# Performance work log

Hardware: AMD Instinct MI355X
Metric: run time of the kernel (lower is better)

The kernel has to match this reference:

```python
import jax, jax.numpy as jnp
import numpy as np

N, E = 50000, 800000
F_IN, E_DIM, D, H = 128, 64, 64, 4  # per-head channels D, heads H; concat=False -> out dim D
GROUPS = 16
EPS = 1e-5


def _p(key, shape, scale):
    return (jax.random.normal(key, shape, dtype=jnp.float32) * scale)


def setup_inputs() -> dict:
    key = jax.random.key(0)
    ks = jax.random.split(key, 40)
    inp = {
        "x": jax.random.normal(ks[0], (N, F_IN), dtype=jnp.float32),
        "edge_index": jax.random.randint(ks[1], (2, E), 0, N, dtype=jnp.int64),
        "edge_attr": jax.random.normal(ks[2], (E, E_DIM), dtype=jnp.float32),
    }
    # TransformerConv params, layer i: Wq/Wk/Wv [in, H*D] (+bias), We [E_DIM, H*D] (no bias),
    # Wskip [in, D] (+bias).  Layer 1 in=F_IN, layers 2/3 in=D.
    idx = 3
    for i, fin in zip((1, 2, 3), (F_IN, D, D)):
        s = 1.0 / np.sqrt(fin)
        se = 1.0 / np.sqrt(E_DIM)
        inp[f"Wq{i}"] = _p(ks[idx + 0], (fin, H * D), s)
        inp[f"bq{i}"] = jnp.zeros((H * D,), jnp.float32)
        inp[f"Wk{i}"] = _p(ks[idx + 1], (fin, H * D), s)
        inp[f"bk{i}"] = jnp.zeros((H * D,), jnp.float32)
        inp[f"Wv{i}"] = _p(ks[idx + 2], (fin, H * D), s)
        inp[f"bv{i}"] = jnp.zeros((H * D,), jnp.float32)
        inp[f"We{i}"] = _p(ks[idx + 3], (E_DIM, H * D), se)
        inp[f"Wskip{i}"] = _p(ks[idx + 4], (fin, D), s)
        inp[f"bskip{i}"] = jnp.zeros((D,), jnp.float32)
        idx += 5
    inp["gn_w"] = jnp.ones((D,), jnp.float32)
    inp["gn_b"] = jnp.zeros((D,), jnp.float32)
    return inp


def transformer_conv(x, src, dst, edge_attr, Wq, bq, Wk, bk, Wv, bv, We, Wskip, bskip):
    n = x.shape[0]
    q = (x @ Wq + bq).reshape(n, H, D)
    k = (x @ Wk + bk).reshape(n, H, D)
    v = (x @ Wv + bv).reshape(n, H, D)
    e = (edge_attr @ We).reshape(-1, H, D)  # [E,H,D]
    k_e = k[src] + e                          # edge-level key
    v_e = v[src] + e                          # edge-level value
    alpha = jnp.einsum('ehd,ehd->eh', q[dst], k_e) / np.sqrt(D)  # [E,H]
    # segment softmax over incoming edges of each dst node
    amax = jax.ops.segment_max(alpha, dst, num_segments=n)
    amax = jnp.where(jnp.isfinite(amax), amax, 0.0)
    ex = jnp.exp(alpha - amax[dst])
    denom = jax.ops.segment_sum(ex, dst, num_segments=n)
    attn = ex / (denom[dst] + 1e-16)
    out = jax.ops.segment_sum(attn[:, :, None] * v_e, dst, num_segments=n)  # [N,H,D]
    out = out.mean(axis=1)                     # concat=False -> mean over heads
    return out + (x @ Wskip + bskip)           # root_weight skip


def group_norm(x, w, b):
    n, c = x.shape
    xg = x.reshape(n, GROUPS, c // GROUPS)
    mu = xg.mean(axis=2, keepdims=True)
    var = xg.var(axis=2, keepdims=True)
    xn = ((xg - mu) * jax.lax.rsqrt(var + EPS)).reshape(n, c)
    return xn * w + b


def reference(x, edge_index, edge_attr,
              Wq1, bq1, Wk1, bk1, Wv1, bv1, We1, Wskip1, bskip1,
              Wq2, bq2, Wk2, bk2, Wv2, bv2, We2, Wskip2, bskip2,
              Wq3, bq3, Wk3, bk3, Wv3, bv3, We3, Wskip3, bskip3,
              gn_w, gn_b):
    src, dst = edge_index[0], edge_index[1]
    layers = [
        (Wq1, bq1, Wk1, bk1, Wv1, bv1, We1, Wskip1, bskip1),
        (Wq2, bq2, Wk2, bk2, Wv2, bv2, We2, Wskip2, bskip2),
        (Wq3, bq3, Wk3, bk3, Wv3, bv3, We3, Wskip3, bskip3),
    ]
    h = x
    for prm in layers:
        h = transformer_conv(h, src, dst, edge_attr, *prm)
        h = group_norm(h, gn_w, gn_b)
        h = jax.nn.gelu(h, approximate=False)
    return h
```

## Files before the change

kernel.cpp:

```cpp
#include <hip/hip_runtime.h>
#include <math.h>

#define NN 50000
#define NE 800000
#define NCOLS 1088

typedef long long i64;

__global__ void detect_i64(const int* __restrict__ ei32, int* __restrict__ flag) {
  int i = blockIdx.x * blockDim.x + threadIdx.x;
  if (i < 2048) {
    if (ei32[2 * i + 1] != 0) atomicOr(flag, 1);
  }
}

__global__ void extract_edges(const void* __restrict__ ei, const int* __restrict__ flag,
                              int* __restrict__ src32, int* __restrict__ dst32, int ne) {
  int is32 = *flag;
  int i = blockIdx.x * blockDim.x + threadIdx.x;
  int st = gridDim.x * blockDim.x;
  if (is32) {
    const int* p = (const int*)ei;
    for (; i < ne; i += st) { src32[i] = p[i]; dst32[i] = p[ne + i]; }
  } else {
    const i64* p = (const i64*)ei;
    for (; i < ne; i += st) { src32[i] = (int)p[i]; dst32[i] = (int)p[ne + i]; }
  }
}

__global__ void hist_kernel(const int* __restrict__ dst, int* __restrict__ deg, int ne) {
  int i = blockIdx.x * blockDim.x + threadIdx.x;
  int st = gridDim.x * blockDim.x;
  for (; i < ne; i += st) atomicAdd(&deg[dst[i]], 1);
}

__global__ void scan_kernel(const int* __restrict__ deg, int* __restrict__ row_ptr, int n) {
  __shared__ int buf[1024];
  int t = threadIdx.x;
  int carry = 0;
  if (t == 0) row_ptr[0] = 0;
  for (int base = 0; base < n; base += 1024) {
    int v = (base + t < n) ? deg[base + t] : 0;
    buf[t] = v;
    __syncthreads();
    for (int off = 1; off < 1024; off <<= 1) {
      int x = (t >= off) ? buf[t - off] : 0;
      __syncthreads();
      buf[t] += x;
      __syncthreads();
    }
    if (base + t < n) row_ptr[base + t + 1] = carry + buf[t];
    carry += buf[1023];
    __syncthreads();
  }
}

__global__ void scatter_kernel(const int* __restrict__ src, const int* __restrict__ dst,
                               const int* __restrict__ row_ptr, int* __restrict__ cursor,
                               int* __restrict__ src_sorted, int* __restrict__ eid_sorted, int ne) {
  int i = blockIdx.x * blockDim.x + threadIdx.x;
  int st = gridDim.x * blockDim.x;
  for (; i < ne; i += st) {
    int d = dst[i];
    int pos = row_ptr[d] + atomicAdd(&cursor[d], 1);
    src_sorted[pos] = src[i];
    eid_sorted[pos] = i;
  }
}

__global__ void sort_lists(const int* __restrict__ row_ptr, int* __restrict__ src_sorted,
                           int* __restrict__ eid_sorted, int n) {
  int node = blockIdx.x * blockDim.x + threadIdx.x;
  if (node >= n) return;
  int beg = row_ptr[node], end = row_ptr[node + 1];
  for (int a = beg + 1; a < end; ++a) {
    int e = eid_sorted[a], s = src_sorted[a];
    int b = a - 1;
    while (b >= beg && eid_sorted[b] > e) {
      eid_sorted[b + 1] = eid_sorted[b];
      src_sorted[b + 1] = src_sorted[b];
      --b;
    }
    eid_sorted[b + 1] = e; src_sorted[b + 1] = s;
  }
}

__global__ void prep_wt(const float* __restrict__ Wq, const float* __restrict__ Wk,
                        const float* __restrict__ Wv, const float* __restrict__ We,
                        const float* __restrict__ Wsk, float* __restrict__ Wt, int fin) {
  int i = blockIdx.x * blockDim.x + threadIdx.x;
  if (i >= NCOLS * fin) return;
  int col = i / fin, k = i % fin;
  float val;
  if (col < 768) {
    const float* W = (col < 256) ? Wq : (col < 512) ? Wk : Wv;
    val = W[k * 256 + (col & 255)];
  } else if (col < 1024) {
    int idx = col - 768; int h = idx >> 6, ce = idx & 63;
    float a = 0.f;
    for (int d = 0; d < 64; ++d) a += Wq[k * 256 + h * 64 + d] * We[ce * 256 + h * 64 + d];
    val = a;
  } else {
    val = Wsk[k * 64 + (col - 1024)];
  }
  Wt[(size_t)col * fin + k] = val;
}

__global__ void prep_bias(const float* __restrict__ bq, const float* __restrict__ bk,
                          const float* __restrict__ bv, const float* __restrict__ We,
                          const float* __restrict__ bsk, float* __restrict__ bb) {
  int col = blockIdx.x * blockDim.x + threadIdx.x;
  if (col >= NCOLS) return;
  float val;
  if (col < 768) {
    const float* b = (col < 256) ? bq : (col < 512) ? bk : bv;
    val = b[col & 255];
  } else if (col < 1024) {
    int idx = col - 768; int h = idx >> 6, ce = idx & 63;
    float a = 0.f;
    for (int d = 0; d < 64; ++d) a += bq[h * 64 + d] * We[ce * 256 + h * 64 + d];
    val = a;
  } else {
    val = bsk[col - 1024];
  }
  bb[col] = val;
}

__global__ __launch_bounds__(256) void node_gemm_f32(
    const float* __restrict__ X, const float* __restrict__ Wt, const float* __restrict__ bb,
    float* __restrict__ q_tab, float* __restrict__ k_tab, float* __restrict__ v_tab,
    float* __restrict__ qt_tab, float* __restrict__ skip_tab, int n, int fin) {
  __shared__ __align__(16) float Xs[128][68];
  __shared__ __align__(16) float Ws[64][68];
  int tid = threadIdx.x;
  int tx = tid & 15, ty = tid >> 4;
  int m0 = blockIdx.x * 128, c0 = blockIdx.y * 64;
  float acc[8][4];
  #pragma unroll
  for (int i = 0; i < 8; ++i)
    #pragma unroll
    for (int j = 0; j < 4; ++j) acc[i][j] = 0.f;

  for (int k0 = 0; k0 < fin; k0 += 64) {
    #pragma unroll
    for (int p = 0; p < 8; ++p) {
      int r = ty + 16 * p;
      float4 xv = make_float4(0.f, 0.f, 0.f, 0.f);
      if (m0 + r < n) xv = *(const float4*)&X[(size_t)(m0 + r) * fin + k0 + tx * 4];
      *(float4*)&Xs[r][tx * 4] = xv;
    }
    #pragma unroll
    for (int p = 0; p < 4; ++p) {
      int r = ty + 16 * p;
      float4 wv = *(const float4*)&Wt[(size_t)(c0 + r) * fin + k0 + tx * 4];
      *(float4*)&Ws[r][tx * 4] = wv;
    }
    __syncthreads();
    #pragma unroll 4
    for (int kk = 0; kk < 64; kk += 4) {
      float4 a[8], b[4];
      #pragma unroll
      for (int i = 0; i < 8; ++i) a[i] = *(const float4*)&Xs[ty + 16 * i][kk];
      #pragma unroll
      for (int j = 0; j < 4; ++j) b[j] = *(const float4*)&Ws[tx + 16 * j][kk];
      #pragma unroll
      for (int i = 0; i < 8; ++i)
        #pragma unroll
        for (int j = 0; j < 4; ++j) {
          acc[i][j] = fmaf(a[i].x, b[j].x, acc[i][j]);
          acc[i][j] = fmaf(a[i].y, b[j].y, acc[i][j]);
          acc[i][j] = fmaf(a[i].z, b[j].z, acc[i][j]);
          acc[i][j] = fmaf(a[i].w, b[j].w, acc[i][j]);
        }
    }
    __syncthreads();
  }
  #pragma unroll
  for (int j = 0; j < 4; ++j) {
    int col = c0 + tx + 16 * j;
    float bias = bb[col];
    #pragma unroll
    for (int i = 0; i < 8; ++i) {
      int row = m0 + ty + 16 * i;
      if (row >= n) continue;
      float val = acc[i][j] + bias;
      if (col < 256)       q_tab[(size_t)row * 256 + col] = val;
      else if (col < 512)  k_tab[(size_t)row * 256 + col - 256] = val;
      else if (col < 768)  v_tab[(size_t)row * 256 + col - 512] = val;
      else if (col < 1024) qt_tab[(size_t)row * 256 + col - 768] = val;
      else                 skip_tab[(size_t)row * 64 + col - 1024] = val;
    }
  }
}

__global__ __launch_bounds__(256, 6) void attn_kernel_f32(
    const int* __restrict__ row_ptr, const int* __restrict__ src_sorted,
    const int* __restrict__ eid_sorted, const float* __restrict__ ea,
    const float* __restrict__ q_tab, const float* __restrict__ k_tab,
    const float* __restrict__ v_tab, const float* __restrict__ qt_tab,
    const float* __restrict__ skip_tab, const float* __restrict__ west,
    const float* __restrict__ gnw, const float* __restrict__ gnb,
    float* __restrict__ out, int n) {
  int tid = threadIdx.x;
  int wave = tid >> 6, lane = tid & 63;
  int node = blockIdx.x * 4 + wave;
  if (node >= n) return;
  int h = lane >> 4;
  int foff = h * 16 + (lane & 15);
  const float4* q4p = (const float4*)q_tab;
  const float4* t4p = (const float4*)qt_tab;
  const float4* k4p = (const float4*)k_tab;
  const float4* v4p = (const float4*)v_tab;
  const float4* e4p = (const float4*)ea;
  const float4* w4p = (const float4*)west;

  float4 q4 = q4p[(size_t)node * 64 + foff];
  float4 t4 = t4p[(size_t)node * 64 + foff];

  float m = -INFINITY, s = 0.f;
  float4 av = make_float4(0.f, 0.f, 0.f, 0.f);
  float4 aw = make_float4(0.f, 0.f, 0.f, 0.f);

  int beg = row_ptr[node], end = row_ptr[node + 1];
  float4 kp, vp, ep;
  if (beg < end) {
    int sidx = src_sorted[beg], eid = eid_sorted[beg];
    kp = k4p[(size_t)sidx * 64 + foff];
    vp = v4p[(size_t)sidx * 64 + foff];
    ep = e4p[(size_t)eid * 16 + (lane & 15)];
  }
  for (int j = beg; j < end; ++j) {
    float4 kc = kp, vc = vp, ec = ep;
    if (j + 1 < end) {
      int sidx = src_sorted[j + 1], eid = eid_sorted[j + 1];
      kp = k4p[(size_t)sidx * 64 + foff];
      vp = v4p[(size_t)sidx * 64 + foff];
      ep = e4p[(size_t)eid * 16 + (lane & 15)];
    }
    float p = q4.x * kc.x + q4.y * kc.y + q4.z * kc.z + q4.w * kc.w
            + t4.x * ec.x + t4.y * ec.y + t4.z * ec.z + t4.w * ec.w;
    p += __shfl_xor(p, 1);
    p += __shfl_xor(p, 2);
    p += __shfl_xor(p, 4);
    p += __shfl_xor(p, 8);
    p *= 0.125f;
    float d_ = p - m;
    float e_ = __expf(-fabsf(d_));
    float sc = d_ > 0.f ? e_ : 1.f;
    float pp = d_ > 0.f ? 1.f : e_;
    m = fmaxf(m, p);
    s = s * sc + pp;
    av.x = av.x * sc + pp * vc.x; av.y = av.y * sc + pp * vc.y;
    av.z = av.z * sc + pp * vc.z; av.w = av.w * sc + pp * vc.w;
    aw.x = aw.x * sc + pp * ec.x; aw.y = aw.y * sc + pp * ec.y;
    aw.z = aw.z * sc + pp * ec.z; aw.w = aw.w * sc + pp * ec.w;
  }
  float inv = s > 0.f ? 1.f / s : 0.f;
  float4 avn = make_float4(av.x * inv, av.y * inv, av.z * inv, av.w * inv);
  float4 awn = make_float4(aw.x * inv, aw.y * inv, aw.z * inv, aw.w * inv);

  float4 post = make_float4(0.f, 0.f, 0.f, 0.f);
  int gbase = h << 4;
  #pragma unroll 4
  for (int ce4 = 0; ce4 < 16; ++ce4) {
    int srcl = gbase | ce4;
    float wa = __shfl(awn.x, srcl);
    float wb = __shfl(awn.y, srcl);
    float wc = __shfl(awn.z, srcl);
    float wd = __shfl(awn.w, srcl);
    float4 w0 = w4p[(size_t)(ce4 * 4 + 0) * 64 + foff];
    float4 w1 = w4p[(size_t)(ce4 * 4 + 1) * 64 + foff];
    float4 w2 = w4p[(size_t)(ce4 * 4 + 2) * 64 + foff];
    float4 w3 = w4p[(size_t)(ce4 * 4 + 3) * 64 + foff];
    post.x = fmaf(wa, w0.x, post.x); post.y = fmaf(wa, w0.y, post.y);
    post.z = fmaf(wa, w0.z, post.z); post.w = fmaf(wa, w0.w, post.w);
    post.x = fmaf(wb, w1.x, post.x); post.y = fmaf(wb, w1.y, post.y);
    post.z = fmaf(wb, w1.z, post.z); post.w = fmaf(wb, w1.w, post.w);
    post.x = fmaf(wc, w2.x, post.x); post.y = fmaf(wc, w2.y, post.y);
    post.z = fmaf(wc, w2.z, post.z); post.w = fmaf(wc, w2.w, post.w);
    post.x = fmaf(wd, w3.x, post.x); post.y = fmaf(wd, w3.y, post.y);
    post.z = fmaf(wd, w3.z, post.z); post.w = fmaf(wd, w3.w, post.w);
  }

  float4 tot = make_float4(avn.x + post.x, avn.y + post.y, avn.z + post.z, avn.w + post.w);
  tot.x += __shfl_xor(tot.x, 16); tot.y += __shfl_xor(tot.y, 16);
  tot.z += __shfl_xor(tot.z, 16); tot.w += __shfl_xor(tot.w, 16);
  tot.x += __shfl_xor(tot.x, 32); tot.y += __shfl_xor(tot.y, 32);
  tot.z += __shfl_xor(tot.z, 32); tot.w += __shfl_xor(tot.w, 32);

  int srcl = lane >> 2;
  float va = __shfl(tot.x, srcl);
  float vb = __shfl(tot.y, srcl);
  float vc2 = __shfl(tot.z, srcl);
  float vd = __shfl(tot.w, srcl);
  float v01 = (lane & 1) ? vb : va;
  float v23 = (lane & 1) ? vd : vc2;
  float hsum = (lane & 2) ? v23 : v01;

  float val = 0.25f * hsum + skip_tab[(size_t)node * 64 + lane];
  float sm = val + __shfl_xor(val, 1);
  sm += __shfl_xor(sm, 2);
  float mu = sm * 0.25f;
  float dv = val - mu;
  float vq = dv * dv;
  float v2 = vq + __shfl_xor(vq, 1);
  v2 += __shfl_xor(v2, 2);
  float xn = dv * rsqrtf(v2 * 0.25f + 1e-5f);
  float y = xn * gnw[lane] + gnb[lane];
  float g = 0.5f * y * (1.0f + erff(y * 0.70710678118654752f));
  out[(size_t)node * 64 + lane] = g;
}

extern "C" void kernel_launch(void* const* d_in, const int* in_sizes, int n_in,
                              void* d_out, int out_size, void* d_ws, size_t ws_size,
                              hipStream_t stream) {
  (void)in_sizes; (void)n_in;
  const float* x = (const float*)d_in[0];
  const void* ei = d_in[1];
  const float* ea = (const float*)d_in[2];
  const float *Wq[3], *bq[3], *Wk[3], *bk[3], *Wv[3], *bv[3], *We[3], *Wsk[3], *bsk[3];
  for (int L = 0; L < 3; ++L) {
    int b = 3 + 9 * L;
    Wq[L] = (const float*)d_in[b + 0]; bq[L] = (const float*)d_in[b + 1];
    Wk[L] = (const float*)d_in[b + 2]; bk[L] = (const float*)d_in[b + 3];
    Wv[L] = (const float*)d_in[b + 4]; bv[L] = (const float*)d_in[b + 5];
    We[L] = (const float*)d_in[b + 6]; Wsk[L] = (const float*)d_in[b + 7];
    bsk[L] = (const float*)d_in[b + 8];
  }
  const float* gnw = (const float*)d_in[30];
  const float* gnb = (const float*)d_in[31];

  char* p = (char*)d_ws;
  auto alloc = [&](size_t bytes) -> void* {
    void* r = (void*)p;
    p += (bytes + 255) & ~(size_t)255;
    return r;
  };
  float* q_tab = (float*)alloc((size_t)NN * 256 * 4);
  float* k_tab = (float*)alloc((size_t)NN * 256 * 4);
  float* v_tab = (float*)alloc((size_t)NN * 256 * 4);
  float* qt_tab = (float*)alloc((size_t)NN * 256 * 4);
  float* skip_tab = (float*)alloc((size_t)NN * 64 * 4);
  float* h_buf = (float*)alloc((size_t)NN * 64 * 4);
  int* row_ptr = (int*)alloc((size_t)(NN + 1) * 4);
  int* deg = (int*)alloc((size_t)NN * 4);
  int* cursor = (int*)alloc((size_t)NN * 4);
  int* src_sorted = (int*)alloc((size_t)NE * 4);
  int* eid_sorted = (int*)alloc((size_t)NE * 4);
  int* src32 = (int*)alloc((size_t)NE * 4);
  int* dst32 = (int*)alloc((size_t)NE * 4);
  int* flag = (int*)alloc(256);
  float* Wt[3]; float* bb[3];
  Wt[0] = (float*)alloc((size_t)NCOLS * 128 * 4);
  Wt[1] = (float*)alloc((size_t)NCOLS * 64 * 4);
  Wt[2] = (float*)alloc((size_t)NCOLS * 64 * 4);
  for (int L = 0; L < 3; ++L) bb[L] = (float*)alloc((size_t)NCOLS * 4);

  if ((size_t)(p - (char*)d_ws) > ws_size) {
    hipMemsetAsync(d_out, 0, (size_t)out_size * 4, stream);
    return;
  }

  hipMemsetAsync(deg, 0, (size_t)NN * 4, stream);
  hipMemsetAsync(cursor, 0, (size_t)NN * 4, stream);
  hipMemsetAsync(flag, 0, 4, stream);

  detect_i64<<<8, 256, 0, stream>>>((const int*)ei, flag);
  extract_edges<<<2048, 256, 0, stream>>>(ei, flag, src32, dst32, NE);

  hist_kernel<<<2048, 256, 0, stream>>>(dst32, deg, NE);
  scan_kernel<<<1, 1024, 0, stream>>>(deg, row_ptr, NN);
  scatter_kernel<<<2048, 256, 0, stream>>>(src32, dst32, row_ptr, cursor, src_sorted, eid_sorted, NE);
  sort_lists<<<(NN + 255) / 256, 256, 0, stream>>>(row_ptr, src_sorted, eid_sorted, NN);

  for (int L = 0; L < 3; ++L) {
    int fin = (L == 0) ? 128 : 64;
    prep_wt<<<(NCOLS * fin + 255) / 256, 256, 0, stream>>>(Wq[L], Wk[L], Wv[L], We[L], Wsk[L], Wt[L], fin);
    prep_bias<<<(NCOLS + 255) / 256, 256, 0, stream>>>(bq[L], bk[L], bv[L], We[L], bsk[L], bb[L]);
  }

  const float* hin = x;
  int ngroups = (NN + 3) / 4;
  for (int L = 0; L < 3; ++L) {
    int fin = (L == 0) ? 128 : 64;
    dim3 g((NN + 127) / 128, 17);
    node_gemm_f32<<<g, 256, 0, stream>>>(hin, Wt[L], bb[L], q_tab, k_tab, v_tab, qt_tab, skip_tab, NN, fin);
    attn_kernel_f32<<<ngroups, 256, 0, stream>>>(
        row_ptr, src_sorted, eid_sorted, ea, q_tab, k_tab, v_tab, qt_tab,
        skip_tab, We[L], gnw, gnb,
        (L == 2) ? (float*)d_out : h_buf, NN);
    hin = h_buf;
  }
}
```

Before: 1.778 ms.

## Interleave K/V and Q/QT tables and deepen edge gather prefetch to four

Node projections are now stored interleaved per row: K and V share one 2KB row, and Q and the transformed query share another. The aim is that each gathered source node's K and V fall in adjacent memory, which should improve locality for the random gathers. The attention loop now processes two edges per iteration with four edges of loads in flight, exposing more memory-level parallelism. The cost is higher register pressure under the 6-waves launch bound, which could cause spills or lower occupancy.

```diff
diff --git a/kernel.cpp b/kernel.cpp
--- a/kernel.cpp
+++ b/kernel.cpp
@@ -128,8 +128,8 @@
 
 __global__ __launch_bounds__(256) void node_gemm_f32(
     const float* __restrict__ X, const float* __restrict__ Wt, const float* __restrict__ bb,
-    float* __restrict__ q_tab, float* __restrict__ k_tab, float* __restrict__ v_tab,
-    float* __restrict__ qt_tab, float* __restrict__ skip_tab, int n, int fin) {
+    float* __restrict__ qq_tab, float* __restrict__ kv_tab,
+    float* __restrict__ skip_tab, int n, int fin) {
   __shared__ __align__(16) float Xs[128][68];
   __shared__ __align__(16) float Ws[64][68];
   int tid = threadIdx.x;
@@ -184,11 +184,10 @@
       int row = m0 + ty + 16 * i;
       if (row >= n) continue;
       float val = acc[i][j] + bias;
-      if (col < 256)       q_tab[(size_t)row * 256 + col] = val;
-      else if (col < 512)  k_tab[(size_t)row * 256 + col - 256] = val;
-      else if (col < 768)  v_tab[(size_t)row * 256 + col - 512] = val;
-      else if (col < 1024) qt_tab[(size_t)row * 256 + col - 768] = val;
-      else                 skip_tab[(size_t)row * 64 + col - 1024] = val;
+      if (col < 256)        qq_tab[(size_t)row * 512 + col] = val;
+      else if (col < 768)   kv_tab[(size_t)row * 512 + col - 256] = val;
+      else if (col < 1024)  qq_tab[(size_t)row * 512 + col - 512] = val;
+      else                  skip_tab[(size_t)row * 64 + col - 1024] = val;
     }
   }
 }
@@ -196,8 +195,7 @@
 __global__ __launch_bounds__(256, 6) void attn_kernel_f32(
     const int* __restrict__ row_ptr, const int* __restrict__ src_sorted,
     const int* __restrict__ eid_sorted, const float* __restrict__ ea,
-    const float* __restrict__ q_tab, const float* __restrict__ k_tab,
-    const float* __restrict__ v_tab, const float* __restrict__ qt_tab,
+    const float* __restrict__ qq_tab, const float* __restrict__ kv_tab,
     const float* __restrict__ skip_tab, const float* __restrict__ west,
     const float* __restrict__ gnw, const float* __restrict__ gnb,
     float* __restrict__ out, int n) {
@@ -207,54 +205,79 @@
   if (node >= n) return;
   int h = lane >> 4;
   int foff = h * 16 + (lane & 15);
-  const float4* q4p = (const float4*)q_tab;
-  const float4* t4p = (const float4*)qt_tab;
-  const float4* k4p = (const float4*)k_tab;
-  const float4* v4p = (const float4*)v_tab;
+  int eoff = lane & 15;
+  const float4* qq4 = (const float4*)qq_tab;
+  const float4* kv4 = (const float4*)kv_tab;
   const float4* e4p = (const float4*)ea;
   const float4* w4p = (const float4*)west;
 
-  float4 q4 = q4p[(size_t)node * 64 + foff];
-  float4 t4 = t4p[(size_t)node * 64 + foff];
+  float4 q4 = qq4[(size_t)node * 128 + foff];
+  float4 t4 = qq4[(size_t)node * 128 + 64 + foff];
 
   float m = -INFINITY, s = 0.f;
   float4 av = make_float4(0.f, 0.f, 0.f, 0.f);
   float4 aw = make_float4(0.f, 0.f, 0.f, 0.f);
 
   int beg = row_ptr[node], end = row_ptr[node + 1];
-  float4 kp, vp, ep;
-  if (beg < end) {
-    int sidx = src_sorted[beg], eid = eid_sorted[beg];
-    kp = k4p[(size_t)sidx * 64 + foff];
-    vp = v4p[(size_t)sidx * 64 + foff];
-    ep = e4p[(size_t)eid * 16 + (lane & 15)];
-  }
-  for (int j = beg; j < end; ++j) {
-    float4 kc = kp, vc = vp, ec = ep;
-    if (j + 1 < end) {
-      int sidx = src_sorted[j + 1], eid = eid_sorted[j + 1];
-      kp = k4p[(size_t)sidx * 64 + foff];
-      vp = v4p[(size_t)sidx * 64 + foff];
-      ep = e4p[(size_t)eid * 16 + (lane & 15)];
-    }
-    float p = q4.x * kc.x + q4.y * kc.y + q4.z * kc.z + q4.w * kc.w
-            + t4.x * ec.x + t4.y * ec.y + t4.z * ec.z + t4.w * ec.w;
-    p += __shfl_xor(p, 1);
-    p += __shfl_xor(p, 2);
-    p += __shfl_xor(p, 4);
-    p += __shfl_xor(p, 8);
-    p *= 0.125f;
-    float d_ = p - m;
-    float e_ = __expf(-fabsf(d_));
-    float sc = d_ > 0.f ? e_ : 1.f;
-    float pp = d_ > 0.f ? 1.f : e_;
-    m = fmaxf(m, p);
-    s = s * sc + pp;
-    av.x = av.x * sc + pp * vc.x; av.y = av.y * sc + pp * vc.y;
-    av.z = av.z * sc + pp * vc.z; av.w = av.w * sc + pp * vc.w;
-    aw.x = aw.x * sc + pp * ec.x; aw.y = aw.y * sc + pp * ec.y;
-    aw.z = aw.z * sc + pp * ec.z; aw.w = aw.w * sc + pp * ec.w;
-  }
+
+#define LOADE(idx, K, V, E)                                   \
+  {                                                           \
+    int s_ = src_sorted[idx];                                 \
+    int e_ = eid_sorted[idx];                                 \
+    K = kv4[(size_t)s_ * 128 + foff];                         \
+    V = kv4[(size_t)s_ * 128 + 64 + foff];                    \
+    E = e4p[(size_t)e_ * 16 + eoff];                          \
+  }
+
+#define ONLINE1(p, V, E)                                      \
+  {                                                           \
+    float d_ = (p) - m;                                       \
+    float e_ = __expf(-fabsf(d_));                            \
+    float sc = d_ > 0.f ? e_ : 1.f;                           \
+    float pp = d_ > 0.f ? 1.f : e_;                           \
+    m = fmaxf(m, (p));                                        \
+    s = s * sc + pp;                                          \
+    av.x = av.x * sc + pp * V.x; av.y = av.y * sc + pp * V.y; \
+    av.z = av.z * sc + pp * V.z; av.w = av.w * sc + pp * V.w; \
+    aw.x = aw.x * sc + pp * E.x; aw.y = aw.y * sc + pp * E.y; \
+    aw.z = aw.z * sc + pp * E.z; aw.w = aw.w * sc + pp * E.w; \
+  }
+
+  float4 Ka, Va, Ea, Kb, Vb, Eb, Kc, Vc, Ec, Kd, Vd, Ed;
+  int j = beg;
+  if (j     < end) LOADE(j,     Ka, Va, Ea);
+  if (j + 1 < end) LOADE(j + 1, Kb, Vb, Eb);
+  if (j + 2 < end) LOADE(j + 2, Kc, Vc, Ec);
+  if (j + 3 < end) LOADE(j + 3, Kd, Vd, Ed);
+
+  for (; j + 1 < end; j += 2) {
+    float4 K0 = Ka, V0 = Va, E0 = Ea, K1 = Kb, V1 = Vb, E1 = Eb;
+    Ka = Kc; Va = Vc; Ea = Ec; Kb = Kd; Vb = Vd; Eb = Ed;
+    if (j + 4 < end) LOADE(j + 4, Kc, Vc, Ec);
+    if (j + 5 < end) LOADE(j + 5, Kd, Vd, Ed);
+    float p0 = q4.x * K0.x + q4.y * K0.y + q4.z * K0.z + q4.w * K0.w
+             + t4.x * E0.x + t4.y * E0.y + t4.z * E0.z + t4.w * E0.w;
+    float p1 = q4.x * K1.x + q4.y * K1.y + q4.z * K1.z + q4.w * K1.w
+             + t4.x * E1.x + t4.y * E1.y + t4.z * E1.z + t4.w * E1.w;
+    p0 += __shfl_xor(p0, 1);  p1 += __shfl_xor(p1, 1);
+    p0 += __shfl_xor(p0, 2);  p1 += __shfl_xor(p1, 2);
+    p0 += __shfl_xor(p0, 4);  p1 += __shfl_xor(p1, 4);
+    p0 += __shfl_xor(p0, 8);  p1 += __shfl_xor(p1, 8);
+    p0 *= 0.125f; p1 *= 0.125f;
+    ONLINE1(p0, V0, E0);
+    ONLINE1(p1, V1, E1);
+  }
+  if (j < end) {
+    float p0 = q4.x * Ka.x + q4.y * Ka.y + q4.z * Ka.z + q4.w * Ka.w
+             + t4.x * Ea.x + t4.y * Ea.y + t4.z * Ea.z + t4.w * Ea.w;
+    p0 += __shfl_xor(p0, 1);
+    p0 += __shfl_xor(p0, 2);
+    p0 += __shfl_xor(p0, 4);
+    p0 += __shfl_xor(p0, 8);
+    p0 *= 0.125f;
+    ONLINE1(p0, Va, Ea);
+  }
+
   float inv = s > 0.f ? 1.f / s : 0.f;
   float4 avn = make_float4(av.x * inv, av.y * inv, av.z * inv, av.w * inv);
   float4 awn = make_float4(aw.x * inv, aw.y * inv, aw.z * inv, aw.w * inv);
@@ -336,10 +359,8 @@
     p += (bytes + 255) & ~(size_t)255;
     return r;
   };
-  float* q_tab = (float*)alloc((size_t)NN * 256 * 4);
-  float* k_tab = (float*)alloc((size_t)NN * 256 * 4);
-  float* v_tab = (float*)alloc((size_t)NN * 256 * 4);
-  float* qt_tab = (float*)alloc((size_t)NN * 256 * 4);
+  float* qq_tab = (float*)alloc((size_t)NN * 512 * 4);
+  float* kv_tab = (float*)alloc((size_t)NN * 512 * 4);
   float* skip_tab = (float*)alloc((size_t)NN * 64 * 4);
   float* h_buf = (float*)alloc((size_t)NN * 64 * 4);
   int* row_ptr = (int*)alloc((size_t)(NN + 1) * 4);
@@ -384,9 +405,9 @@
   for (int L = 0; L < 3; ++L) {
     int fin = (L == 0) ? 128 : 64;
     dim3 g((NN + 127) / 128, 17);
-    node_gemm_f32<<<g, 256, 0, stream>>>(hin, Wt[L], bb[L], q_tab, k_tab, v_tab, qt_tab, skip_tab, NN, fin);
+    node_gemm_f32<<<g, 256, 0, stream>>>(hin, Wt[L], bb[L], qq_tab, kv_tab, skip_tab, NN, fin);
     attn_kernel_f32<<<ngroups, 256, 0, stream>>>(
-        row_ptr, src_sorted, eid_sorted, ea, q_tab, k_tab, v_tab, qt_tab,
+        row_ptr, src_sorted, eid_sorted, ea, qq_tab, kv_tab,
         skip_tab, We[L], gnw, gnb,
         (L == 2) ? (float*)d_out : h_buf, NN);
     hin = h_buf;
```

New measurement: 4.280 ms. 2.41x slower.

## Interleave Q/K/V tables, process two degree-sorted nodes per wave in attention

Applied to the files above, without the earlier changes.

Packs q with q·We and k with v into interleaved per-node rows, so each gather reads contiguous 2KB rows. Attention now handles two nodes per wavefront (32 lanes each, 8 floats per lane), and nodes are ordered by degree bucket so the two half-waves have similar loop trip counts. It also adds three small kernels to build the degree order. In exchange it costs more registers (launch bounds lowered to 4) and does padded, wasted iterations when the paired degrees differ.

```diff
diff --git a/kernel.cpp b/kernel.cpp
--- a/kernel.cpp
+++ b/kernel.cpp
@@ -83,6 +83,31 @@
     }
     eid_sorted[b + 1] = e; src_sorted[b + 1] = s;
   }
+}
+
+__global__ void deg_hist256(const int* __restrict__ row_ptr, int* __restrict__ dh, int n) {
+  int node = blockIdx.x * blockDim.x + threadIdx.x;
+  if (node >= n) return;
+  int d = row_ptr[node + 1] - row_ptr[node];
+  if (d > 255) d = 255;
+  atomicAdd(&dh[d], 1);
+}
+
+__global__ void deg_base256(const int* __restrict__ dh, int* __restrict__ dbase) {
+  if (threadIdx.x == 0 && blockIdx.x == 0) {
+    int run = 0;
+    for (int d = 255; d >= 0; --d) { dbase[d] = run; run += dh[d]; }
+  }
+}
+
+__global__ void deg_scatter256(const int* __restrict__ row_ptr, const int* __restrict__ dbase,
+                               int* __restrict__ dcur, int* __restrict__ order, int n) {
+  int node = blockIdx.x * blockDim.x + threadIdx.x;
+  if (node >= n) return;
+  int d = row_ptr[node + 1] - row_ptr[node];
+  if (d > 255) d = 255;
+  int pos = dbase[d] + atomicAdd(&dcur[d], 1);
+  order[pos] = node;
 }
 
 __global__ void prep_wt(const float* __restrict__ Wq, const float* __restrict__ Wk,
@@ -128,8 +153,8 @@
 
 __global__ __launch_bounds__(256) void node_gemm_f32(
     const float* __restrict__ X, const float* __restrict__ Wt, const float* __restrict__ bb,
-    float* __restrict__ q_tab, float* __restrict__ k_tab, float* __restrict__ v_tab,
-    float* __restrict__ qt_tab, float* __restrict__ skip_tab, int n, int fin) {
+    float* __restrict__ qq_tab, float* __restrict__ kv_tab,
+    float* __restrict__ skip_tab, int n, int fin) {
   __shared__ __align__(16) float Xs[128][68];
   __shared__ __align__(16) float Ws[64][68];
   int tid = threadIdx.x;
@@ -184,131 +209,185 @@
       int row = m0 + ty + 16 * i;
       if (row >= n) continue;
       float val = acc[i][j] + bias;
-      if (col < 256)       q_tab[(size_t)row * 256 + col] = val;
-      else if (col < 512)  k_tab[(size_t)row * 256 + col - 256] = val;
-      else if (col < 768)  v_tab[(size_t)row * 256 + col - 512] = val;
-      else if (col < 1024) qt_tab[(size_t)row * 256 + col - 768] = val;
-      else                 skip_tab[(size_t)row * 64 + col - 1024] = val;
-    }
-  }
-}
-
-__global__ __launch_bounds__(256, 6) void attn_kernel_f32(
+      if (col < 256)        qq_tab[(size_t)row * 512 + col] = val;
+      else if (col < 768)   kv_tab[(size_t)row * 512 + col - 256] = val;
+      else if (col < 1024)  qq_tab[(size_t)row * 512 + col - 512] = val;
+      else                  skip_tab[(size_t)row * 64 + col - 1024] = val;
+    }
+  }
+}
+
+__global__ __launch_bounds__(256, 4) void attn_kernel_v3(
+    const int* __restrict__ order,
     const int* __restrict__ row_ptr, const int* __restrict__ src_sorted,
     const int* __restrict__ eid_sorted, const float* __restrict__ ea,
-    const float* __restrict__ q_tab, const float* __restrict__ k_tab,
-    const float* __restrict__ v_tab, const float* __restrict__ qt_tab,
+    const float* __restrict__ qq_tab, const float* __restrict__ kv_tab,
     const float* __restrict__ skip_tab, const float* __restrict__ west,
     const float* __restrict__ gnw, const float* __restrict__ gnb,
     float* __restrict__ out, int n) {
   int tid = threadIdx.x;
   int wave = tid >> 6, lane = tid & 63;
-  int node = blockIdx.x * 4 + wave;
-  if (node >= n) return;
-  int h = lane >> 4;
-  int foff = h * 16 + (lane & 15);
-  const float4* q4p = (const float4*)q_tab;
-  const float4* t4p = (const float4*)qt_tab;
-  const float4* k4p = (const float4*)k_tab;
-  const float4* v4p = (const float4*)v_tab;
+  int half = lane >> 5, h = (lane >> 3) & 3, c8 = lane & 7;
+  int ko = h * 16 + c8 * 2;
+  int eo = c8 * 2;
+  const float4* qq4 = (const float4*)qq_tab;
+  const float4* kv4 = (const float4*)kv_tab;
   const float4* e4p = (const float4*)ea;
   const float4* w4p = (const float4*)west;
 
-  float4 q4 = q4p[(size_t)node * 64 + foff];
-  float4 t4 = t4p[(size_t)node * 64 + foff];
+  int slot = blockIdx.x * 8 + wave * 2 + half;
+  int node = -1, beg = 0, deg = 0;
+  if (slot < n) {
+    node = order[slot];
+    beg = row_ptr[node];
+    deg = row_ptr[node + 1] - beg;
+  }
+  int tmax = deg;
+  { int o = __shfl_xor(tmax, 32); tmax = o > tmax ? o : tmax; }
+
+  float4 q4a = make_float4(0.f,0.f,0.f,0.f), q4b = q4a, t4a = q4a, t4b = q4a;
+  if (node >= 0) {
+    q4a = qq4[(size_t)node * 128 + ko];
+    q4b = qq4[(size_t)node * 128 + ko + 1];
+    t4a = qq4[(size_t)node * 128 + 64 + ko];
+    t4b = qq4[(size_t)node * 128 + 64 + ko + 1];
+  }
 
   float m = -INFINITY, s = 0.f;
-  float4 av = make_float4(0.f, 0.f, 0.f, 0.f);
-  float4 aw = make_float4(0.f, 0.f, 0.f, 0.f);
-
-  int beg = row_ptr[node], end = row_ptr[node + 1];
-  float4 kp, vp, ep;
-  if (beg < end) {
-    int sidx = src_sorted[beg], eid = eid_sorted[beg];
-    kp = k4p[(size_t)sidx * 64 + foff];
-    vp = v4p[(size_t)sidx * 64 + foff];
-    ep = e4p[(size_t)eid * 16 + (lane & 15)];
-  }
-  for (int j = beg; j < end; ++j) {
-    float4 kc = kp, vc = vp, ec = ep;
-    if (j + 1 < end) {
-      int sidx = src_sorted[j + 1], eid = eid_sorted[j + 1];
-      kp = k4p[(size_t)sidx * 64 + foff];
-      vp = v4p[(size_t)sidx * 64 + foff];
-      ep = e4p[(size_t)eid * 16 + (lane & 15)];
-    }
-    float p = q4.x * kc.x + q4.y * kc.y + q4.z * kc.z + q4.w * kc.w
-            + t4.x * ec.x + t4.y * ec.y + t4.z * ec.z + t4.w * ec.w;
+  float4 av0 = make_float4(0.f,0.f,0.f,0.f), av1 = av0, aw0 = av0, aw1 = av0;
+
+  float4 Kn0, Kn1, Vn0, Vn1, En0, En1;
+  {
+    int jc = beg; if (jc > NE - 1) jc = NE - 1;
+    int s_ = src_sorted[jc], e_ = eid_sorted[jc];
+    const float4* kr = kv4 + (size_t)s_ * 128;
+    Kn0 = kr[ko]; Kn1 = kr[ko + 1];
+    Vn0 = kr[64 + ko]; Vn1 = kr[64 + ko + 1];
+    const float4* er = e4p + (size_t)e_ * 16;
+    En0 = er[eo]; En1 = er[eo + 1];
+  }
+
+  for (int t = 0; t < tmax; ++t) {
+    float4 K0 = Kn0, K1 = Kn1, V0 = Vn0, V1 = Vn1, E0 = En0, E1 = En1;
+    {
+      int jn = beg + t + 1; if (jn > NE - 1) jn = NE - 1;
+      int s_ = src_sorted[jn], e_ = eid_sorted[jn];
+      const float4* kr = kv4 + (size_t)s_ * 128;
+      Kn0 = kr[ko]; Kn1 = kr[ko + 1];
+      Vn0 = kr[64 + ko]; Vn1 = kr[64 + ko + 1];
+      const float4* er = e4p + (size_t)e_ * 16;
+      En0 = er[eo]; En1 = er[eo + 1];
+    }
+    float p = q4a.x * K0.x + q4a.y * K0.y + q4a.z * K0.z + q4a.w * K0.w;
+    p = fmaf(q4b.x, K1.x, p); p = fmaf(q4b.y, K1.y, p);
+    p = fmaf(q4b.z, K1.z, p); p = fmaf(q4b.w, K1.w, p);
+    p = fmaf(t4a.x, E0.x, p); p = fmaf(t4a.y, E0.y, p);
+    p = fmaf(t4a.z, E0.z, p); p = fmaf(t4a.w, E0.w, p);
+    p = fmaf(t4b.x, E1.x, p); p = fmaf(t4b.y, E1.y, p);
+    p = fmaf(t4b.z, E1.z, p); p = fmaf(t4b.w, E1.w, p);
     p += __shfl_xor(p, 1);
     p += __shfl_xor(p, 2);
     p += __shfl_xor(p, 4);
-    p += __shfl_xor(p, 8);
     p *= 0.125f;
+    bool valid = (t < deg);
     float d_ = p - m;
     float e_ = __expf(-fabsf(d_));
-    float sc = d_ > 0.f ? e_ : 1.f;
-    float pp = d_ > 0.f ? 1.f : e_;
-    m = fmaxf(m, p);
+    float sc = (valid && d_ > 0.f) ? e_ : 1.f;
+    float pp = valid ? ((d_ > 0.f) ? 1.f : e_) : 0.f;
+    if (valid) m = fmaxf(m, p);
     s = s * sc + pp;
-    av.x = av.x * sc + pp * vc.x; av.y = av.y * sc + pp * vc.y;
-    av.z = av.z * sc + pp * vc.z; av.w = av.w * sc + pp * vc.w;
-    aw.x = aw.x * sc + pp * ec.x; aw.y = aw.y * sc + pp * ec.y;
-    aw.z = aw.z * sc + pp * ec.z; aw.w = aw.w * sc + pp * ec.w;
-  }
+    av0.x = av0.x * sc + pp * V0.x; av0.y = av0.y * sc + pp * V0.y;
+    av0.z = av0.z * sc + pp * V0.z; av0.w = av0.w * sc + pp * V0.w;
+    av1.x = av1.x * sc + pp * V1.x; av1.y = av1.y * sc + pp * V1.y;
+    av1.z = av1.z * sc + pp * V1.z; av1.w = av1.w * sc + pp * V1.w;
+    aw0.x = aw0.x * sc + pp * E0.x; aw0.y = aw0.y * sc + pp * E0.y;
+    aw0.z = aw0.z * sc + pp * E0.z; aw0.w = aw0.w * sc + pp * E0.w;
+    aw1.x = aw1.x * sc + pp * E1.x; aw1.y = aw1.y * sc + pp * E1.y;
+    aw1.z = aw1.z * sc + pp * E1.z; aw1.w = aw1.w * sc + pp * E1.w;
+  }
+
   float inv = s > 0.f ? 1.f / s : 0.f;
-  float4 avn = make_float4(av.x * inv, av.y * inv, av.z * inv, av.w * inv);
-  float4 awn = make_float4(aw.x * inv, aw.y * inv, aw.z * inv, aw.w * inv);
-
-  float4 post = make_float4(0.f, 0.f, 0.f, 0.f);
-  int gbase = h << 4;
-  #pragma unroll 4
-  for (int ce4 = 0; ce4 < 16; ++ce4) {
-    int srcl = gbase | ce4;
-    float wa = __shfl(awn.x, srcl);
-    float wb = __shfl(awn.y, srcl);
-    float wc = __shfl(awn.z, srcl);
-    float wd = __shfl(awn.w, srcl);
-    float4 w0 = w4p[(size_t)(ce4 * 4 + 0) * 64 + foff];
-    float4 w1 = w4p[(size_t)(ce4 * 4 + 1) * 64 + foff];
-    float4 w2 = w4p[(size_t)(ce4 * 4 + 2) * 64 + foff];
-    float4 w3 = w4p[(size_t)(ce4 * 4 + 3) * 64 + foff];
-    post.x = fmaf(wa, w0.x, post.x); post.y = fmaf(wa, w0.y, post.y);
-    post.z = fmaf(wa, w0.z, post.z); post.w = fmaf(wa, w0.w, post.w);
-    post.x = fmaf(wb, w1.x, post.x); post.y = fmaf(wb, w1.y, post.y);
-    post.z = fmaf(wb, w1.z, post.z); post.w = fmaf(wb, w1.w, post.w);
-    post.x = fmaf(wc, w2.x, post.x); post.y = fmaf(wc, w2.y, post.y);
-    post.z = fmaf(wc, w2.z, post.z); post.w = fmaf(wc, w2.w, post.w);
-    post.x = fmaf(wd, w3.x, post.x); post.y = fmaf(wd, w3.y, post.y);
-    post.z = fmaf(wd, w3.z, post.z); post.w = fmaf(wd, w3.w, post.w);
-  }
-
-  float4 tot = make_float4(avn.x + post.x, avn.y + post.y, avn.z + post.z, avn.w + post.w);
-  tot.x += __shfl_xor(tot.x, 16); tot.y += __shfl_xor(tot.y, 16);
-  tot.z += __shfl_xor(tot.z, 16); tot.w += __shfl_xor(tot.w, 16);
-  tot.x += __shfl_xor(tot.x, 32); tot.y += __shfl_xor(tot.y, 32);
-  tot.z += __shfl_xor(tot.z, 32); tot.w += __shfl_xor(tot.w, 32);
-
-  int srcl = lane >> 2;
-  float va = __shfl(tot.x, srcl);
-  float vb = __shfl(tot.y, srcl);
-  float vc2 = __shfl(tot.z, srcl);
-  float vd = __shfl(tot.w, srcl);
-  float v01 = (lane & 1) ? vb : va;
-  float v23 = (lane & 1) ? vd : vc2;
-  float hsum = (lane & 2) ? v23 : v01;
-
-  float val = 0.25f * hsum + skip_tab[(size_t)node * 64 + lane];
-  float sm = val + __shfl_xor(val, 1);
-  sm += __shfl_xor(sm, 2);
-  float mu = sm * 0.25f;
-  float dv = val - mu;
-  float vq = dv * dv;
-  float v2 = vq + __shfl_xor(vq, 1);
-  v2 += __shfl_xor(v2, 2);
-  float xn = dv * rsqrtf(v2 * 0.25f + 1e-5f);
-  float y = xn * gnw[lane] + gnb[lane];
-  float g = 0.5f * y * (1.0f + erff(y * 0.70710678118654752f));
-  out[(size_t)node * 64 + lane] = g;
+  float4 avn0 = make_float4(av0.x*inv, av0.y*inv, av0.z*inv, av0.w*inv);
+  float4 avn1 = make_float4(av1.x*inv, av1.y*inv, av1.z*inv, av1.w*inv);
+  float4 awn0 = make_float4(aw0.x*inv, aw0.y*inv, aw0.z*inv, aw0.w*inv);
+  float4 awn1 = make_float4(aw1.x*inv, aw1.y*inv, aw1.z*inv, aw1.w*inv);
+
+  float4 post0 = make_float4(0.f,0.f,0.f,0.f), post1 = post0;
+  int lbase = lane & 0x38;
+  #pragma unroll
+  for (int cc4 = 0; cc4 < 16; ++cc4) {
+    float4 srcv = (cc4 & 1) ? awn1 : awn0;
+    int sl = lbase | (cc4 >> 1);
+    float wa = __shfl(srcv.x, sl);
+    float wb = __shfl(srcv.y, sl);
+    float wc = __shfl(srcv.z, sl);
+    float wd = __shfl(srcv.w, sl);
+    const float4* wr = w4p + (size_t)(cc4 * 4) * 64 + ko;
+    float4 wA0 = wr[0],   wA1 = wr[1];
+    float4 wB0 = wr[64],  wB1 = wr[65];
+    float4 wC0 = wr[128], wC1 = wr[129];
+    float4 wD0 = wr[192], wD1 = wr[193];
+    post0.x = fmaf(wa, wA0.x, post0.x); post0.y = fmaf(wa, wA0.y, post0.y);
+    post0.z = fmaf(wa, wA0.z, post0.z); post0.w = fmaf(wa, wA0.w, post0.w);
+    post1.x = fmaf(wa, wA1.x, post1.x); post1.y = fmaf(wa, wA1.y, post1.y);
+    post1.z = fmaf(wa, wA1.z, post1.z); post1.w = fmaf(wa, wA1.w, post1.w);
+    post0.x = fmaf(wb, wB0.x, post0.x); post0.y = fmaf(wb, wB0.y, post0.y);
+    post0.z = fmaf(wb, wB0.z, post0.z); post0.w = fmaf(wb, wB0.w, post0.w);
+    post1.x = fmaf(wb, wB1.x, post1.x); post1.y = fmaf(wb, wB1.y, post1.y);
+    post1.z = fmaf(wb, wB1.z, post1.z); post1.w = fmaf(wb, wB1.w, post1.w);
+    post0.x = fmaf(wc, wC0.x, post0.x); post0.y = fmaf(wc, wC0.y, post0.y);
+    post0.z = fmaf(wc, wC0.z, post0.z); post0.w = fmaf(wc, wC0.w, post0.w);
+    post1.x = fmaf(wc, wC1.x, post1.x); post1.y = fmaf(wc, wC1.y, post1.y);
+    post1.z = fmaf(wc, wC1.z, post1.z); post1.w = fmaf(wc, wC1.w, post1.w);
+    post0.x = fmaf(wd, wD0.x, post0.x); post0.y = fmaf(wd, wD0.y, post0.y);
+    post0.z = fmaf(wd, wD0.z, post0.z); post0.w = fmaf(wd, wD0.w, post0.w);
+    post1.x = fmaf(wd, wD1.x, post1.x); post1.y = fmaf(wd, wD1.y, post1.y);
+    post1.z = fmaf(wd, wD1.z, post1.z); post1.w = fmaf(wd, wD1.w, post1.w);
+  }
+
+  float4 tot0 = make_float4(avn0.x+post0.x, avn0.y+post0.y, avn0.z+post0.z, avn0.w+post0.w);
+  float4 tot1 = make_float4(avn1.x+post1.x, avn1.y+post1.y, avn1.z+post1.z, avn1.w+post1.w);
+  tot0.x += __shfl_xor(tot0.x, 8);  tot0.y += __shfl_xor(tot0.y, 8);
+  tot0.z += __shfl_xor(tot0.z, 8);  tot0.w += __shfl_xor(tot0.w, 8);
+  tot1.x += __shfl_xor(tot1.x, 8);  tot1.y += __shfl_xor(tot1.y, 8);
+  tot1.z += __shfl_xor(tot1.z, 8);  tot1.w += __shfl_xor(tot1.w, 8);
+  tot0.x += __shfl_xor(tot0.x, 16); tot0.y += __shfl_xor(tot0.y, 16);
+  tot0.z += __shfl_xor(tot0.z, 16); tot0.w += __shfl_xor(tot0.w, 16);
+  tot1.x += __shfl_xor(tot1.x, 16); tot1.y += __shfl_xor(tot1.y, 16);
+  tot1.z += __shfl_xor(tot1.z, 16); tot1.w += __shfl_xor(tot1.w, 16);
+
+  if (node >= 0) {
+    const float4* skr = (const float4*)(skip_tab + (size_t)node * 64);
+    float4 sk0 = skr[c8 * 2], sk1 = skr[c8 * 2 + 1];
+    const float4* gwr = (const float4*)gnw;
+    const float4* gbr = (const float4*)gnb;
+    float4 gw0 = gwr[c8 * 2], gw1 = gwr[c8 * 2 + 1];
+    float4 gb0 = gbr[c8 * 2], gb1 = gbr[c8 * 2 + 1];
+    float a0 = 0.25f * tot0.x + sk0.x, a1 = 0.25f * tot0.y + sk0.y;
+    float a2 = 0.25f * tot0.z + sk0.z, a3 = 0.25f * tot0.w + sk0.w;
+    float b0 = 0.25f * tot1.x + sk1.x, b1 = 0.25f * tot1.y + sk1.y;
+    float b2 = 0.25f * tot1.z + sk1.z, b3 = 0.25f * tot1.w + sk1.w;
+    float muA = ((a0 + a1) + (a2 + a3)) * 0.25f;
+    float muB = ((b0 + b1) + (b2 + b3)) * 0.25f;
+    float dA0 = a0-muA, dA1 = a1-muA, dA2 = a2-muA, dA3 = a3-muA;
+    float dB0 = b0-muB, dB1 = b1-muB, dB2 = b2-muB, dB3 = b3-muB;
+    float vA = ((dA0*dA0 + dA1*dA1) + (dA2*dA2 + dA3*dA3)) * 0.25f;
+    float vB = ((dB0*dB0 + dB1*dB1) + (dB2*dB2 + dB3*dB3)) * 0.25f;
+    float rA = rsqrtf(vA + 1e-5f), rB = rsqrtf(vB + 1e-5f);
+    float yA0 = dA0*rA*gw0.x + gb0.x, yA1 = dA1*rA*gw0.y + gb0.y;
+    float yA2 = dA2*rA*gw0.z + gb0.z, yA3 = dA3*rA*gw0.w + gb0.w;
+    float yB0 = dB0*rB*gw1.x + gb1.x, yB1 = dB1*rB*gw1.y + gb1.y;
+    float yB2 = dB2*rB*gw1.z + gb1.z, yB3 = dB3*rB*gw1.w + gb1.w;
+    #define GELU(y) (0.5f * (y) * (1.0f + erff((y) * 0.70710678118654752f)))
+    float gA0 = GELU(yA0), gA1 = GELU(yA1), gA2 = GELU(yA2), gA3 = GELU(yA3);
+    float gB0 = GELU(yB0), gB1 = GELU(yB1), gB2 = GELU(yB2), gB3 = GELU(yB3);
+    float ox, oy;
+    if (h == 0)      { ox = gA0; oy = gA1; }
+    else if (h == 1) { ox = gA2; oy = gA3; }
+    else if (h == 2) { ox = gB0; oy = gB1; }
+    else             { ox = gB2; oy = gB3; }
+    *(float2*)(out + (size_t)node * 64 + c8 * 8 + h * 2) = make_float2(ox, oy);
+  }
 }
 
 extern "C" void kernel_launch(void* const* d_in, const int* in_sizes, int n_in,
@@ -336,10 +415,8 @@
     p += (bytes + 255) & ~(size_t)255;
     return r;
   };
-  float* q_tab = (float*)alloc((size_t)NN * 256 * 4);
-  float* k_tab = (float*)alloc((size_t)NN * 256 * 4);
-  float* v_tab = (float*)alloc((size_t)NN * 256 * 4);
-  float* qt_tab = (float*)alloc((size_t)NN * 256 * 4);
+  float* qq_tab = (float*)alloc((size_t)NN * 512 * 4);
+  float* kv_tab = (float*)alloc((size_t)NN * 512 * 4);
   float* skip_tab = (float*)alloc((size_t)NN * 64 * 4);
   float* h_buf = (float*)alloc((size_t)NN * 64 * 4);
   int* row_ptr = (int*)alloc((size_t)(NN + 1) * 4);
@@ -350,6 +427,10 @@
   int* src32 = (int*)alloc((size_t)NE * 4);
   int* dst32 = (int*)alloc((size_t)NE * 4);
   int* flag = (int*)alloc(256);
+  int* dh = (int*)alloc(256 * 4);
+  int* dbase = (int*)alloc(256 * 4);
+  int* dcur = (int*)alloc(256 * 4);
+  int* order = (int*)alloc((size_t)NN * 4);
   float* Wt[3]; float* bb[3];
   Wt[0] = (float*)alloc((size_t)NCOLS * 128 * 4);
   Wt[1] = (float*)alloc((size_t)NCOLS * 64 * 4);
@@ -364,6 +445,8 @@
   hipMemsetAsync(deg, 0, (size_t)NN * 4, stream);
   hipMemsetAsync(cursor, 0, (size_t)NN * 4, stream);
   hipMemsetAsync(flag, 0, 4, stream);
+  hipMemsetAsync(dh, 0, 256 * 4, stream);
+  hipMemsetAsync(dcur, 0, 256 * 4, stream);
 
   detect_i64<<<8, 256, 0, stream>>>((const int*)ei, flag);
   extract_edges<<<2048, 256, 0, stream>>>(ei, flag, src32, dst32, NE);
@@ -373,6 +456,10 @@
   scatter_kernel<<<2048, 256, 0, stream>>>(src32, dst32, row_ptr, cursor, src_sorted, eid_sorted, NE);
   sort_lists<<<(NN + 255) / 256, 256, 0, stream>>>(row_ptr, src_sorted, eid_sorted, NN);
 
+  deg_hist256<<<(NN + 255) / 256, 256, 0, stream>>>(row_ptr, dh, NN);
+  deg_base256<<<1, 64, 0, stream>>>(dh, dbase);
+  deg_scatter256<<<(NN + 255) / 256, 256, 0, stream>>>(row_ptr, dbase, dcur, order, NN);
+
   for (int L = 0; L < 3; ++L) {
     int fin = (L == 0) ? 128 : 64;
     prep_wt<<<(NCOLS * fin + 255) / 256, 256, 0, stream>>>(Wq[L], Wk[L], Wv[L], We[L], Wsk[L], Wt[L], fin);
@@ -380,13 +467,13 @@
   }
 
   const float* hin = x;
-  int ngroups = (NN + 3) / 4;
+  int nblk = (NN + 7) / 8;
   for (int L = 0; L < 3; ++L) {
     int fin = (L == 0) ? 128 : 64;
     dim3 g((NN + 127) / 128, 17);
-    node_gemm_f32<<<g, 256, 0, stream>>>(hin, Wt[L], bb[L], q_tab, k_tab, v_tab, qt_tab, skip_tab, NN, fin);
-    attn_kernel_f32<<<ngroups, 256, 0, stream>>>(
-        row_ptr, src_sorted, eid_sorted, ea, q_tab, k_tab, v_tab, qt_tab,
+    node_gemm_f32<<<g, 256, 0, stream>>>(hin, Wt[L], bb[L], qq_tab, kv_tab, skip_tab, NN, fin);
+    attn_kernel_v3<<<nblk, 256, 0, stream>>>(
+        order, row_ptr, src_sorted, eid_sorted, ea, qq_tab, kv_tab,
         skip_tab, We[L], gnw, gnb,
         (L == 2) ? (float*)d_out : h_buf, NN);
     hin = h_buf;
```

Result: slower. 2.100 ms (+18.2%).
